# Optimization experiments

Measured on AMD Instinct MI355X. Metric: run time of the kernel, lower is better.

## Reference

```python
import jax, jax.numpy as jnp
import numpy as np

B, H, W, C, S, ITERS = 32, 80, 80, 32, 9, 3
HW = H * W
SCALE = C ** -0.5


def _grid(h, w):
    # matches SoftPositionEmbedding.build_grid: [1, h, w, 4] = [g, 1-g]
    r = jnp.stack(jnp.meshgrid(jnp.linspace(0., 1., h), jnp.linspace(0., 1., w), indexing='ij'), -1)
    return jnp.concatenate([r, 1. - r], -1)[None].astype(jnp.float32)


def _ln(x, g, b, ax):
    m = x.mean(ax, keepdims=True)
    v = x.var(ax, keepdims=True)
    return (x - m) / jnp.sqrt(v + 1e-5) * g + b


def _conv(x, w, b, p):
    y = jax.lax.conv_general_dilated(x, w, (1, 1), [(p, p), (p, p)],
                                     dimension_numbers=('NCHW', 'OIHW', 'NCHW'))
    return y + b[None, :, None, None]


def _convT(x, w, b, p):
    # stride-1 ConvTranspose2d == conv with spatially flipped kernel, pad k-1-p; w is [I,O,kh,kw]
    k = w.shape[-1]
    q = k - 1 - p
    y = jax.lax.conv_general_dilated(x, jnp.flip(w, (2, 3)), (1, 1), [(q, q), (q, q)],
                                     dimension_numbers=('NCHW', 'IOHW', 'NCHW'))
    return y + b[None, :, None, None]


def setup_inputs() -> dict:
    key = jax.random.key(0)
    ks = iter(jax.random.split(key, 64))

    def n(sh, s=0.05):
        return jax.random.normal(next(ks), sh, jnp.float32) * s

    return dict(
        x=jax.random.normal(next(ks), (B, 1, H, W), jnp.float32),
        slot_noise=jax.random.normal(next(ks), (B, S, C), jnp.float32),
        enc_w1=n((C, 1, 5, 5)), enc_b1=jnp.zeros((C,)),
        enc_w2=n((C, C, 5, 5)), enc_b2=jnp.zeros((C,)),
        enc_w3=n((C, C, 5, 5)), enc_b3=jnp.zeros((C,)),
        enc_w4=n((C, C, 5, 5)), enc_b4=jnp.zeros((C,)),
        pe_enc_w=n((C, 4)), pe_enc_b=jnp.zeros((C,)),
        ln_enc_g=jnp.ones((HW, C)), ln_enc_b=jnp.zeros((HW, C)),
        mlp_w1=n((C, C)), mlp_b1=jnp.zeros((C,)),
        mlp_w2=n((C, C)), mlp_b2=jnp.zeros((C,)),
        slots_mu=n((1, 1, C), 1.0), slots_sigma=jnp.abs(n((1, 1, C), 1.0)),
        ni_g=jnp.ones((C,)), ni_b=jnp.zeros((C,)),
        ns_g=jnp.ones((C,)), ns_b=jnp.zeros((C,)),
        q_w=n((C, C)), q_b=jnp.zeros((C,)),
        k_w=n((C, C)), k_b=jnp.zeros((C,)),
        v_w=n((C, C)), v_b=jnp.zeros((C,)),
        gru_wih=n((3 * C, C)), gru_whh=n((3 * C, C)),
        gru_bih=jnp.zeros((3 * C,)), gru_bhh=jnp.zeros((3 * C,)),
        res_ln_g=jnp.ones((C,)), res_ln_b=jnp.zeros((C,)),
        res_w1=n((C, C)), res_b1=jnp.zeros((C,)),
        res_w2=n((C, C)), res_b2=jnp.zeros((C,)),
        pe_dec_w=n((C, 4)), pe_dec_b=jnp.zeros((C,)),
        dec_w1=n((C, C, 5, 5)), dec_b1=jnp.zeros((C,)),
        dec_w2=n((C, C, 5, 5)), dec_b2=jnp.zeros((C,)),
        dec_w3=n((C, C, 5, 5)), dec_b3=jnp.zeros((C,)),
        dec_w4=n((C, 2, 3, 3)), dec_b4=jnp.zeros((2,)),
    )


def _forward(x, slot_noise, enc_w1, enc_b1, enc_w2, enc_b2, enc_w3, enc_b3, enc_w4, enc_b4,
             pe_enc_w, pe_enc_b, ln_enc_g, ln_enc_b, mlp_w1, mlp_b1, mlp_w2, mlp_b2,
             slots_mu, slots_sigma, ni_g, ni_b, ns_g, ns_b, q_w, q_b, k_w, k_b, v_w, v_b,
             gru_wih, gru_whh, gru_bih, gru_bhh, res_ln_g, res_ln_b, res_w1, res_b1,
             res_w2, res_b2, pe_dec_w, pe_dec_b, dec_w1, dec_b1, dec_w2, dec_b2,
             dec_w3, dec_b3, dec_w4, dec_b4):
    grid = _grid(H, W)  # [1,H,W,4]
    # --- conv encoder ---
    h = jax.nn.relu(_conv(x, enc_w1, enc_b1, 2))
    h = jax.nn.relu(_conv(h, enc_w2, enc_b2, 2))
    h = jax.nn.relu(_conv(h, enc_w3, enc_b3, 2))
    h = jax.nn.relu(_conv(h, enc_w4, enc_b4, 2))
    h = h.transpose(0, 2, 3, 1) + (grid @ pe_enc_w.T + pe_enc_b)  # soft pos emb
    h = h.reshape(B, HW, C)
    h = _ln(h, ln_enc_g, ln_enc_b, (-2, -1))  # LayerNorm([HW, C]): joint over last 2 dims
    h = jax.nn.relu(h @ mlp_w1.T + mlp_b1) @ mlp_w2.T + mlp_b2
    # --- slot attention ---
    slots = slots_mu + slots_sigma * slot_noise  # torch.normal(mu, sigma)
    xn = _ln(h, ni_g, ni_b, -1)
    keys = xn @ k_w.T + k_b
    values = xn @ v_w.T + v_b
    attn = None
    for _ in range(ITERS):
        prev = slots
        sn = _ln(slots, ns_g, ns_b, -1)
        q = sn @ q_w.T + q_b
        dots = jnp.einsum('bid,bjd->bij', q, keys) * SCALE  # [B,S,HW]
        attn = jax.nn.softmax(dots, axis=1) + 1e-8  # softmax over slots
        attn = attn / attn.sum(-1, keepdims=True)
        upd = jnp.einsum('bjd,bij->bid', values, attn)  # [B,S,C]
        # PyTorch GRUCell
        u2 = upd.reshape(-1, C)
        h2 = prev.reshape(-1, C)
        gx = u2 @ gru_wih.T + gru_bih
        gh = h2 @ gru_whh.T + gru_bhh
        xr, xz, xc = jnp.split(gx, 3, -1)
        hr, hz, hc = jnp.split(gh, 3, -1)
        r = jax.nn.sigmoid(xr + hr)
        z = jax.nn.sigmoid(xz + hz)
        cand = jnp.tanh(xc + r * hc)
        slots = ((1. - z) * cand + z * h2).reshape(B, S, C)
        res = _ln(slots, res_ln_g, res_ln_b, -1)
        res = jax.nn.relu(res @ res_w1.T + res_b1) @ res_w2.T + res_b2
        slots = slots + res
    # --- spatial-broadcast decoder ---
    d = jnp.broadcast_to(slots.reshape(B * S, 1, 1, C), (B * S, H, W, C))
    d = d + (grid @ pe_dec_w.T + pe_dec_b)
    d = d.transpose(0, 3, 1, 2)
    d = jax.nn.relu(_convT(d, dec_w1, dec_b1, 2))
    d = jax.nn.relu(_convT(d, dec_w2, dec_b2, 2))
    d = jax.nn.relu(_convT(d, dec_w3, dec_b3, 2))
    d = _convT(d, dec_w4, dec_b4, 1)
    d = d.transpose(0, 2, 3, 1).reshape(B, S, H, W, 2)
    recon, mlog = d[..., :1], d[..., 1:]
    mask = jax.nn.softmax(mlog, axis=1)  # over slots
    combined = (recon * mask).sum(1).transpose(0, 3, 1, 2)  # [B,1,H,W]
    return (combined, recon.transpose(0, 1, 4, 2, 3), mask.transpose(0, 1, 4, 2, 3),
            slots, attn.reshape(B, S, 1, H, W))


def reference(x, slot_noise, enc_w1, enc_b1, enc_w2, enc_b2, enc_w3, enc_b3, enc_w4, enc_b4,
              pe_enc_w, pe_enc_b, ln_enc_g, ln_enc_b, mlp_w1, mlp_b1, mlp_w2, mlp_b2,
              slots_mu, slots_sigma, ni_g, ni_b, ns_g, ns_b, q_w, q_b, k_w, k_b, v_w, v_b,
              gru_wih, gru_whh, gru_bih, gru_bhh, res_ln_g, res_ln_b, res_w1, res_b1,
              res_w2, res_b2, pe_dec_w, pe_dec_b, dec_w1, dec_b1, dec_w2, dec_b2,
              dec_w3, dec_b3, dec_w4, dec_b4):
    return _forward(x, slot_noise, enc_w1, enc_b1, enc_w2, enc_b2, enc_w3, enc_b3, enc_w4, enc_b4,
                    pe_enc_w, pe_enc_b, ln_enc_g, ln_enc_b, mlp_w1, mlp_b1, mlp_w2, mlp_b2,
                    slots_mu, slots_sigma, ni_g, ni_b, ns_g, ns_b, q_w, q_b, k_w, k_b, v_w, v_b,
                    gru_wih, gru_whh, gru_bih, gru_bhh, res_ln_g, res_ln_b, res_w1, res_b1,
                    res_w2, res_b2, pe_dec_w, pe_dec_b, dec_w1, dec_b1, dec_w2, dec_b2,
                    dec_w3, dec_b3, dec_w4, dec_b4)
```

## Files before the change

### kernel.cpp

```cpp
#include <hip/hip_runtime.h>
#include <cstddef>
#include <cstdint>


namespace {

constexpr int Bb  = 32;
constexpr int HWp = 6400;
constexpr float SCALEf = 0.17677669529663687f;

constexpr size_t O_COMB  = 0;
constexpr size_t O_RECON = 204800;
constexpr size_t O_MASK  = 2048000;
constexpr size_t O_SLOTS = 3891200;
constexpr size_t O_ATTN  = 3900416;

constexpr size_t W_PEENC = 0;
constexpr size_t W_PEDEC = 204800;
constexpr size_t W_BASE  = 409600;
constexpr size_t W_TC    = 512000;
constexpr size_t W_TS    = 537600;
constexpr size_t W_WP    = 768000;
constexpr size_t W_WPM   = 844800;
constexpr size_t W_LNPART= 846848;
constexpr size_t W_MEANR = 848448;
constexpr size_t W_Q     = 848512;
constexpr size_t W_SLOTS = 857728;
constexpr size_t W_APART = 866944;
constexpr size_t W_RSUM  = 874144;
constexpr size_t W_UP2   = 874432;
constexpr size_t W_KEYS  = 1104832;
constexpr size_t W_VALS  = 4381632;
constexpr size_t W_POOL  = 7658432;
constexpr size_t W_TOTAL = 29115328;

typedef __attribute__((ext_vector_type(8))) short short8;
typedef __attribute__((ext_vector_type(4))) float f32x4;

__device__ __forceinline__ ushort f2bf(float f) {
  uint u = __builtin_bit_cast(uint, f);
  uint r = (u + 0x7fffu + ((u >> 16) & 1u)) >> 16;
  return (ushort)r;
}
__device__ __forceinline__ float bf2f(ushort b) {
  uint u = ((uint)b) << 16;
  return __builtin_bit_cast(float, u);
}
__device__ __forceinline__ void unpk2(uint w, float& a, float& b) {
  a = __builtin_bit_cast(float, w << 16);
  b = __builtin_bit_cast(float, w & 0xffff0000u);
}

__device__ __forceinline__ float lane_ln(float v, int o, const float* __restrict__ g,
                                         const float* __restrict__ b) {
  float s = v;
#pragma unroll
  for (int m = 16; m >= 1; m >>= 1) s += __shfl_xor(s, m);
  float mean = s * (1.f / 32.f);
  float d = v - mean;
  float q = d * d;
#pragma unroll
  for (int m = 16; m >= 1; m >>= 1) q += __shfl_xor(q, m);
  float rstd = rsqrtf(q * (1.f / 32.f) + 1e-5f);
  return d * rstd * g[o] + b[o];
}


__global__ void k_pe_maps(const float* __restrict__ pew_e, const float* __restrict__ peb_e,
                          const float* __restrict__ pew_d, const float* __restrict__ peb_d,
                          float* __restrict__ pe_enc, float* __restrict__ pe_dec) {
  int hw = blockIdx.x * 256 + threadIdx.x;
  if (hw >= HWp) return;
  int y = hw / 80, x = hw % 80;
  float g0 = y * (1.f / 79.f), g1 = x * (1.f / 79.f);
  float g2 = 1.f - g0, g3 = 1.f - g1;
#pragma unroll
  for (int c = 0; c < 32; ++c) {
    pe_enc[(size_t)hw * 32 + c] = peb_e[c] + g0 * pew_e[c * 4] + g1 * pew_e[c * 4 + 1] +
                                  g2 * pew_e[c * 4 + 2] + g3 * pew_e[c * 4 + 3];
    pe_dec[(size_t)c * HWp + hw] = peb_d[c] + g0 * pew_d[c * 4] + g1 * pew_d[c * 4 + 1] +
                                   g2 * pew_d[c * 4 + 2] + g3 * pew_d[c * 4 + 3];
  }
}


__global__ void k_pack(const float* __restrict__ w, ushort* __restrict__ dst, int trans) {
  int tap = blockIdx.x;
  int grp = threadIdx.x >> 6, lane = threadIdx.x & 63;
  int ky = tap / 5, kx = tap % 5;
  int m = grp * 16 + (lane & 15);
  int kb = (lane >> 4) * 8;
  ushort* o = dst + ((size_t)(tap * 2 + grp) * 64 + lane) * 8;
#pragma unroll
  for (int j = 0; j < 8; ++j) {
    int k = kb + j;
    float v = trans ? w[(size_t)k * 800 + m * 25 + (4 - ky) * 5 + (4 - kx)]
                    : w[(size_t)m * 800 + k * 25 + ky * 5 + kx];
    o[j] = f2bf(v);
  }
}

__global__ void k_pack_mat(const float* __restrict__ w, ushort* __restrict__ dst) {
  int grp = threadIdx.x >> 6, lane = threadIdx.x & 63;
  int m = grp * 16 + (lane & 15), kb = (lane >> 4) * 8;
  ushort* o = dst + ((size_t)(grp * 64 + lane)) * 8;
#pragma unroll
  for (int j = 0; j < 8; ++j) o[j] = f2bf(w[m * 32 + kb + j]);
}


__global__ void k_prep_tc(const float* __restrict__ w, float* __restrict__ tc) {
  const int rep[5] = {0, 1, 40, 78, 79};
  int cls = blockIdx.x;
  int yc = cls / 5, xc = cls % 5;
  int ci = threadIdx.x >> 5, co = threadIdx.x & 31;
  int yr = rep[yc], xr = rep[xc];
  float s = 0.f;
#pragma unroll
  for (int ky = 0; ky < 5; ++ky) {
    if ((unsigned)(yr + ky - 2) >= 80u) continue;
#pragma unroll
    for (int kx = 0; kx < 5; ++kx) {
      if ((unsigned)(xr + kx - 2) >= 80u) continue;
      s += w[(size_t)ci * 800 + co * 25 + (4 - ky) * 5 + (4 - kx)];
    }
  }
  tc[(size_t)cls * 1024 + ci * 32 + co] = s;
}

__global__ void k_ts(const float* __restrict__ tc, const float* __restrict__ slots,
                     float* __restrict__ ts) {
  int idx = blockIdx.x * 256 + threadIdx.x;
  if (idx >= 288 * 800) return;
  int img = idx / 800, rem = idx % 800;
  int cls = rem >> 5, o = rem & 31;
  float s = 0.f;
#pragma unroll
  for (int ci = 0; ci < 32; ++ci)
    s += tc[(size_t)cls * 1024 + ci * 32 + o] * slots[(size_t)img * 32 + ci];
  ts[idx] = s;
}


template <int MODE, bool RELU>
__global__ __launch_bounds__(256, 4) void k_conv_mfma(
    const void* __restrict__ in_, const ushort* __restrict__ wp,
    const float* __restrict__ bias, ushort* __restrict__ out_,
    const float* __restrict__ ts, int n0) {
  __shared__ int4 sm[1600];
  const int n = blockIdx.y;
  const int ty = blockIdx.x / 5, tx = blockIdx.x % 5;
  const int t = threadIdx.x;

  for (int i = t; i < 1600; i += 256) {
    int u = i & 3, px = i >> 2;
    int x = px % 20, r = px / 20;
    int gy = ty * 16 + r - 2, gx = tx * 16 + x - 2;
    int4 pk = {0, 0, 0, 0};
    if ((unsigned)gy < 80u && (unsigned)gx < 80u) {
      int hw = gy * 80 + gx;
      if constexpr (MODE == 0) {
        const float* fp = (const float*)in_;
        ushort bb[8];
#pragma unroll
        for (int j = 0; j < 8; ++j)
          bb[j] = f2bf(fp[(size_t)(u * 8 + j) * HWp + hw]);
        pk.x = (int)((uint)bb[0] | ((uint)bb[1] << 16));
        pk.y = (int)((uint)bb[2] | ((uint)bb[3] << 16));
        pk.z = (int)((uint)bb[4] | ((uint)bb[5] << 16));
        pk.w = (int)((uint)bb[6] | ((uint)bb[7] << 16));
      } else if constexpr (MODE == 1) {
        pk = *(const int4*)((const ushort*)in_ + ((size_t)n * HWp + hw) * 32 + u * 8);
      } else {
        int4 bp = *(const int4*)((const ushort*)in_ + (size_t)hw * 32 + u * 8);
        int yc = gy < 2 ? gy : (gy > 77 ? gy - 75 : 2);
        int xc = gx < 2 ? gx : (gx > 77 ? gx - 75 : 2);
        const float* tp = ts + ((size_t)(n0 + n) * 25 + (yc * 5 + xc)) * 32 + u * 8;
        float t0, t1;
        uint* pw = (uint*)&pk;
        const uint* bw = (const uint*)&bp;
#pragma unroll
        for (int h = 0; h < 4; ++h) {
          unpk2(bw[h], t0, t1);
          float f0 = fmaxf(t0 + tp[2 * h], 0.f);
          float f1 = fmaxf(t1 + tp[2 * h + 1], 0.f);
          pw[h] = (uint)f2bf(f0) | ((uint)f2bf(f1) << 16);
        }
      }
    }
    int up = u ^ ((x >> 1) & 3);
    sm[(r * 20 + x) * 4 + up] = pk;
  }
  __syncthreads();

  const int wv = t >> 6, lane = t & 63;
  const int l15 = lane & 15, lg = lane >> 4;
  const short8* smS = (const short8*)sm;

  f32x4 acc[4][2];
#pragma unroll
  for (int o = 0; o < 4; ++o)
#pragma unroll
    for (int c = 0; c < 2; ++c) acc[o][c] = f32x4{0.f, 0.f, 0.f, 0.f};

#pragma unroll
  for (int dx = 0; dx < 5; ++dx) {
    short8 Adx[5][2];
#pragma unroll
    for (int dy = 0; dy < 5; ++dy) {
      int tap = dy * 5 + dx;
      Adx[dy][0] = *(const short8*)(wp + ((size_t)(tap * 2 + 0) * 64 + lane) * 8);
      Adx[dy][1] = *(const short8*)(wp + ((size_t)(tap * 2 + 1) * 64 + lane) * 8);
    }
    const int xx = l15 + dx;
    const int us = lg ^ ((xx >> 1) & 3);
#pragma unroll
    for (int r8 = 0; r8 < 8; ++r8) {
      short8 Bv = smS[((wv * 4 + r8) * 20 + xx) * 4 + us];
#pragma unroll
      for (int o = 0; o < 4; ++o) {
        int dy = r8 - o;
        if (dy < 0 || dy > 4) continue;
        acc[o][0] = __builtin_amdgcn_mfma_f32_16x16x32_bf16(Adx[dy][0], Bv, acc[o][0], 0, 0, 0);
        acc[o][1] = __builtin_amdgcn_mfma_f32_16x16x32_bf16(Adx[dy][1], Bv, acc[o][1], 0, 0, 0);
      }
    }
  }

  float bv[2][4];
#pragma unroll
  for (int cg = 0; cg < 2; ++cg)
#pragma unroll
    for (int q = 0; q < 4; ++q) bv[cg][q] = bias[cg * 16 + lg * 4 + q];
  const int ybase = ty * 16 + wv * 4, xbase = tx * 16 + l15;
#pragma unroll
  for (int o = 0; o < 4; ++o) {
    size_t px = (size_t)n * HWp + (ybase + o) * 80 + xbase;
#pragma unroll
    for (int cg = 0; cg < 2; ++cg) {
      f32x4 v = acc[o][cg];
      float o0 = v[0] + bv[cg][0], o1 = v[1] + bv[cg][1];
      float o2 = v[2] + bv[cg][2], o3 = v[3] + bv[cg][3];
      if (RELU) {
        o0 = fmaxf(o0, 0.f); o1 = fmaxf(o1, 0.f);
        o2 = fmaxf(o2, 0.f); o3 = fmaxf(o3, 0.f);
      }
      uint2 pk;
      pk.x = (uint)f2bf(o0) | ((uint)f2bf(o1) << 16);
      pk.y = (uint)f2bf(o2) | ((uint)f2bf(o3) << 16);
      *(uint2*)(out_ + px * 32 + cg * 16 + lg * 4) = pk;
    }
  }
}


__global__ __launch_bounds__(256) void k_conv1(const float* __restrict__ in,
                                               const float* __restrict__ w,
                                               const float* __restrict__ b,
                                               ushort* __restrict__ out) {
  int hw = blockIdx.x * 256 + threadIdx.x;
  int n = blockIdx.y;
  int y = hw / 80, x = hw % 80;
  float xv[25];
#pragma unroll
  for (int ky = 0; ky < 5; ++ky)
#pragma unroll
    for (int kx = 0; kx < 5; ++kx) {
      int iy = y + ky - 2, ix = x + kx - 2;
      xv[ky * 5 + kx] = ((unsigned)iy < 80u && (unsigned)ix < 80u)
                            ? in[(size_t)n * HWp + iy * 80 + ix] : 0.f;
    }
  float a[32];
#pragma unroll
  for (int co = 0; co < 32; ++co) {
    float s = b[co];
#pragma unroll
    for (int tp = 0; tp < 25; ++tp) s = fmaf(xv[tp], w[co * 25 + tp], s);
    a[co] = fmaxf(s, 0.f);
  }
  ushort* op = out + ((size_t)n * HWp + hw) * 32;
#pragma unroll
  for (int g = 0; g < 4; ++g) {
    uint4 pk;
    pk.x = (uint)f2bf(a[g * 8 + 0]) | ((uint)f2bf(a[g * 8 + 1]) << 16);
    pk.y = (uint)f2bf(a[g * 8 + 2]) | ((uint)f2bf(a[g * 8 + 3]) << 16);
    pk.z = (uint)f2bf(a[g * 8 + 4]) | ((uint)f2bf(a[g * 8 + 5]) << 16);
    pk.w = (uint)f2bf(a[g * 8 + 6]) | ((uint)f2bf(a[g * 8 + 7]) << 16);
    *(uint4*)(op + g * 8) = pk;
  }
}


__global__ __launch_bounds__(256) void k_conv4(const ushort* __restrict__ in,
                                               const float* __restrict__ w,
                                               const float* __restrict__ b,
                                               float* __restrict__ outR,
                                               float* __restrict__ outM, int n0) {
  __shared__ float sw[2 * 288];
  for (int e = threadIdx.x; e < 576; e += 256) {
    int co = e / 288, rem = e % 288;
    int tap = rem / 32, ci = rem % 32;
    sw[e] = w[(size_t)(ci * 2 + co) * 9 + 8 - tap];
  }
  __syncthreads();
  int hw = blockIdx.x * 256 + threadIdx.x;
  int nl = blockIdx.y;
  int y = hw / 80, x = hw % 80;
  float a0 = b[0], a1 = b[1];
  const ushort* ip = in + (size_t)nl * HWp * 32;
#pragma unroll
  for (int ky = 0; ky < 3; ++ky) {
#pragma unroll
    for (int kx = 0; kx < 3; ++kx) {
      int iy = y + ky - 1, ix = x + kx - 1;
      if ((unsigned)iy >= 80u || (unsigned)ix >= 80u) continue;
      int tap = ky * 3 + kx;
      const int4* p = (const int4*)(ip + (size_t)(iy * 80 + ix) * 32);
      const float* w0 = sw + tap * 32;
      const float* w1 = sw + 288 + tap * 32;
#pragma unroll
      for (int u = 0; u < 4; ++u) {
        int4 ch = p[u];
        const uint* cw = (const uint*)&ch;
#pragma unroll
        for (int h = 0; h < 4; ++h) {
          float v0, v1;
          unpk2(cw[h], v0, v1);
          int ci = u * 8 + h * 2;
          a0 = fmaf(v0, w0[ci], a0);     a1 = fmaf(v0, w1[ci], a1);
          a0 = fmaf(v1, w0[ci + 1], a0); a1 = fmaf(v1, w1[ci + 1], a1);
        }
      }
    }
  }
  outR[(size_t)(n0 + nl) * HWp + hw] = a0;
  outM[(size_t)(n0 + nl) * HWp + hw] = a1;
}


__global__ __launch_bounds__(256) void k_hstats(const ushort* __restrict__ enc,
                                                const float* __restrict__ pe_enc,
                                                float* __restrict__ lnpart) {
  int b = blockIdx.y;
  int hw = blockIdx.x * 256 + threadIdx.x;
  const int4* ep = (const int4*)(enc + ((size_t)b * HWp + hw) * 32);
  float v[32];
#pragma unroll
  for (int u = 0; u < 4; ++u) {
    int4 ch = ep[u];
    const uint* cw = (const uint*)&ch;
#pragma unroll
    for (int h = 0; h < 4; ++h) unpk2(cw[h], v[u * 8 + h * 2], v[u * 8 + h * 2 + 1]);
  }
  float s = 0.f, ss = 0.f;
#pragma unroll
  for (int c = 0; c < 32; ++c) {
    v[c] += pe_enc[(size_t)hw * 32 + c];
    s += v[c]; ss += v[c] * v[c];
  }
  __shared__ float r1[256], r2[256];
  r1[threadIdx.x] = s; r2[threadIdx.x] = ss;
  __syncthreads();
  for (int off = 128; off > 0; off >>= 1) {
    if (threadIdx.x < off) { r1[threadIdx.x] += r1[threadIdx.x + off]; r2[threadIdx.x] += r2[threadIdx.x + off]; }
    __syncthreads();
  }
  if (threadIdx.x == 0) {
    lnpart[(size_t)(b * 25 + blockIdx.x) * 2] = r1[0];
    lnpart[(size_t)(b * 25 + blockIdx.x) * 2 + 1] = r2[0];
  }
}

__global__ void k_statsfin(const float* __restrict__ lnpart, float* __restrict__ meanr) {
  int b = threadIdx.x;
  if (b >= 32) return;
  float s = 0.f, ss = 0.f;
  for (int k = 0; k < 25; ++k) {
    s += lnpart[(size_t)(b * 25 + k) * 2];
    ss += lnpart[(size_t)(b * 25 + k) * 2 + 1];
  }
  float m = s * (1.f / 204800.f);
  float var = ss * (1.f / 204800.f) - m * m;
  meanr[b * 2] = m;
  meanr[b * 2 + 1] = rsqrtf(var + 1e-5f);
}


__global__ __launch_bounds__(256) void k_lnmlpkv_mfma(
    const ushort* __restrict__ enc, const float* __restrict__ pe,
    const float* __restrict__ meanr,
    const float* __restrict__ g, const float* __restrict__ bb,
    const ushort* __restrict__ wm,
    const float* __restrict__ b1, const float* __restrict__ b2,
    const float* __restrict__ nig, const float* __restrict__ nib,
    const float* __restrict__ kb, const float* __restrict__ vb,
    ushort* __restrict__ keys, ushort* __restrict__ vals) {
  __shared__ ushort ls[256 * 32];
  const int b = blockIdx.y, jb = blockIdx.x;
  const int t = threadIdx.x, wv = t >> 6, lane = t & 63;
  const int l15 = lane & 15, lg = lane >> 4;
  const int skey = l15 & 3;

  short8 A[4][2];
#pragma unroll
  for (int mt = 0; mt < 4; ++mt)
#pragma unroll
    for (int gr = 0; gr < 2; ++gr)
      A[mt][gr] = *(const short8*)(wm + ((size_t)(mt * 2 + gr) * 64 + lane) * 8);

  float4 b1v0 = *(const float4*)(b1 + lg * 4),  b1v1 = *(const float4*)(b1 + 16 + lg * 4);
  float4 b2v0 = *(const float4*)(b2 + lg * 4),  b2v1 = *(const float4*)(b2 + 16 + lg * 4);
  float4 ng0  = *(const float4*)(nig + lg * 4), ng1  = *(const float4*)(nig + 16 + lg * 4);
  float4 nb0  = *(const float4*)(nib + lg * 4), nb1  = *(const float4*)(nib + 16 + lg * 4);
  float4 kbv0 = *(const float4*)(kb + lg * 4),  kbv1 = *(const float4*)(kb + 16 + lg * 4);
  float4 vbv0 = *(const float4*)(vb + lg * 4),  vbv1 = *(const float4*)(vb + 16 + lg * 4);

  const float m_ = meanr[b * 2], rs_ = meanr[b * 2 + 1];

  short8 bx[4];
#pragma unroll
  for (int g2 = 0; g2 < 4; ++g2) {
    int pos = jb * 256 + wv * 64 + g2 * 16 + l15;
    int4 e = *(const int4*)(enc + ((size_t)b * HWp + pos) * 32 + lg * 8);
    float xv[8];
    const uint* ew = (const uint*)&e;
#pragma unroll
    for (int h = 0; h < 4; ++h) unpk2(ew[h], xv[2 * h], xv[2 * h + 1]);
    float4 p0 = *(const float4*)(pe + (size_t)pos * 32 + lg * 8);
    float4 p1 = *(const float4*)(pe + (size_t)pos * 32 + lg * 8 + 4);
    float4 g0 = *(const float4*)(g + (size_t)pos * 32 + lg * 8);
    float4 g1 = *(const float4*)(g + (size_t)pos * 32 + lg * 8 + 4);
    float4 q0 = *(const float4*)(bb + (size_t)pos * 32 + lg * 8);
    float4 q1 = *(const float4*)(bb + (size_t)pos * 32 + lg * 8 + 4);
    float pv[8] = {p0.x, p0.y, p0.z, p0.w, p1.x, p1.y, p1.z, p1.w};
    float gv[8] = {g0.x, g0.y, g0.z, g0.w, g1.x, g1.y, g1.z, g1.w};
    float qv[8] = {q0.x, q0.y, q0.z, q0.w, q1.x, q1.y, q1.z, q1.w};
    uint pk[4];
#pragma unroll
    for (int h = 0; h < 4; ++h) {
      float f0 = (xv[2 * h] + pv[2 * h] - m_) * rs_ * gv[2 * h] + qv[2 * h];
      float f1 = (xv[2 * h + 1] + pv[2 * h + 1] - m_) * rs_ * gv[2 * h + 1] + qv[2 * h + 1];
      pk[h] = (uint)f2bf(f0) | ((uint)f2bf(f1) << 16);
    }
    bx[g2] = __builtin_bit_cast(short8, *(int4*)pk);
  }

  auto lds_write = [&](int posl, int cg, const f32x4& v) {
    int u = cg * 2 + (lg >> 1);
    int us = u ^ skey;
    uint2 pk;
    pk.x = (uint)f2bf(v[0]) | ((uint)f2bf(v[1]) << 16);
    pk.y = (uint)f2bf(v[2]) | ((uint)f2bf(v[3]) << 16);
    *(uint2*)(ls + (size_t)posl * 32 + us * 8 + (lg & 1) * 4) = pk;
  };

#pragma unroll
  for (int g2 = 0; g2 < 4; ++g2) {
    int posl = wv * 64 + g2 * 16 + l15;
    f32x4 a0 = __builtin_amdgcn_mfma_f32_16x16x32_bf16(A[0][0], bx[g2], f32x4{0, 0, 0, 0}, 0, 0, 0);
    f32x4 a1 = __builtin_amdgcn_mfma_f32_16x16x32_bf16(A[0][1], bx[g2], f32x4{0, 0, 0, 0}, 0, 0, 0);
    f32x4 r0, r1;
#pragma unroll
    for (int q = 0; q < 4; ++q) {
      r0[q] = fmaxf(a0[q] + (&b1v0.x)[q], 0.f);
      r1[q] = fmaxf(a1[q] + (&b1v1.x)[q], 0.f);
    }
    lds_write(posl, 0, r0);
    lds_write(posl, 1, r1);
  }
  __syncthreads();
  short8 t0f[4];
#pragma unroll
  for (int g2 = 0; g2 < 4; ++g2) {
    int posl = wv * 64 + g2 * 16 + l15;
    t0f[g2] = *(const short8*)(ls + (size_t)posl * 32 + (lg ^ skey) * 8);
  }
  __syncthreads();

#pragma unroll
  for (int g2 = 0; g2 < 4; ++g2) {
    int posl = wv * 64 + g2 * 16 + l15;
    f32x4 c0 = __builtin_amdgcn_mfma_f32_16x16x32_bf16(A[1][0], t0f[g2], f32x4{0, 0, 0, 0}, 0, 0, 0);
    f32x4 c1 = __builtin_amdgcn_mfma_f32_16x16x32_bf16(A[1][1], t0f[g2], f32x4{0, 0, 0, 0}, 0, 0, 0);
#pragma unroll
    for (int q = 0; q < 4; ++q) { c0[q] += (&b2v0.x)[q]; c1[q] += (&b2v1.x)[q]; }
    float s = 0.f;
#pragma unroll
    for (int q = 0; q < 4; ++q) s += c0[q] + c1[q];
    s += __shfl_xor(s, 16); s += __shfl_xor(s, 32);
    float mean = s * (1.f / 32.f);
    float var = 0.f;
#pragma unroll
    for (int q = 0; q < 4; ++q) {
      float d0 = c0[q] - mean, d1 = c1[q] - mean;
      var += d0 * d0 + d1 * d1;
    }
    var += __shfl_xor(var, 16); var += __shfl_xor(var, 32);
    float rstd = rsqrtf(var * (1.f / 32.f) + 1e-5f);
    f32x4 y0, y1;
#pragma unroll
    for (int q = 0; q < 4; ++q) {
      y0[q] = (c0[q] - mean) * rstd * (&ng0.x)[q] + (&nb0.x)[q];
      y1[q] = (c1[q] - mean) * rstd * (&ng1.x)[q] + (&nb1.x)[q];
    }
    lds_write(posl, 0, y0);
    lds_write(posl, 1, y1);
  }
  __syncthreads();
  short8 xnf[4];
#pragma unroll
  for (int g2 = 0; g2 < 4; ++g2) {
    int posl = wv * 64 + g2 * 16 + l15;
    xnf[g2] = *(const short8*)(ls + (size_t)posl * 32 + (lg ^ skey) * 8);
  }

#pragma unroll
  for (int g2 = 0; g2 < 4; ++g2) {
    int pos = jb * 256 + wv * 64 + g2 * 16 + l15;
    size_t px = ((size_t)b * HWp + pos) * 32;
    f32x4 k0 = __builtin_amdgcn_mfma_f32_16x16x32_bf16(A[2][0], xnf[g2], f32x4{0, 0, 0, 0}, 0, 0, 0);
    f32x4 k1 = __builtin_amdgcn_mfma_f32_16x16x32_bf16(A[2][1], xnf[g2], f32x4{0, 0, 0, 0}, 0, 0, 0);
    f32x4 v0 = __builtin_amdgcn_mfma_f32_16x16x32_bf16(A[3][0], xnf[g2], f32x4{0, 0, 0, 0}, 0, 0, 0);
    f32x4 v1 = __builtin_amdgcn_mfma_f32_16x16x32_bf16(A[3][1], xnf[g2], f32x4{0, 0, 0, 0}, 0, 0, 0);
    uint2 pk;
    pk.x = (uint)f2bf(k0[0] + kbv0.x) | ((uint)f2bf(k0[1] + kbv0.y) << 16);
    pk.y = (uint)f2bf(k0[2] + kbv0.z) | ((uint)f2bf(k0[3] + kbv0.w) << 16);
    *(uint2*)(keys + px + lg * 4) = pk;
    pk.x = (uint)f2bf(k1[0] + kbv1.x) | ((uint)f2bf(k1[1] + kbv1.y) << 16);
    pk.y = (uint)f2bf(k1[2] + kbv1.z) | ((uint)f2bf(k1[3] + kbv1.w) << 16);
    *(uint2*)(keys + px + 16 + lg * 4) = pk;
    pk.x = (uint)f2bf(v0[0] + vbv0.x) | ((uint)f2bf(v0[1] + vbv0.y) << 16);
    pk.y = (uint)f2bf(v0[2] + vbv0.z) | ((uint)f2bf(v0[3] + vbv0.w) << 16);
    *(uint2*)(vals + px + lg * 4) = pk;
    pk.x = (uint)f2bf(v1[0] + vbv1.x) | ((uint)f2bf(v1[1] + vbv1.y) << 16);
    pk.y = (uint)f2bf(v1[2] + vbv1.z) | ((uint)f2bf(v1[3] + vbv1.w) << 16);
    *(uint2*)(vals + px + 16 + lg * 4) = pk;
  }
}


__global__ __launch_bounds__(256) void k_init_q(
    const float* __restrict__ mu, const float* __restrict__ sig,
    const float* __restrict__ noise,
    const float* __restrict__ nsg, const float* __restrict__ nsb,
    const float* __restrict__ qw, const float* __restrict__ qb,
    float* __restrict__ slots, float* __restrict__ qbuf) {
  int rl = threadIdx.x >> 5, o = threadIdx.x & 31;
  int r = blockIdx.x * 8 + rl;
  float s = mu[o] + sig[o] * noise[(size_t)r * 32 + o];
  slots[(size_t)r * 32 + o] = s;
  float y = lane_ln(s, o, nsg, nsb);
  __shared__ float S[8][32];
  S[rl][o] = y;
  __syncthreads();
  float qv = qb[o];
#pragma unroll
  for (int c = 0; c < 32; ++c) qv = fmaf(S[rl][c], qw[o * 32 + c], qv);
  qbuf[(size_t)r * 32 + o] = qv;
}

template <bool LAST>
__global__ __launch_bounds__(256) void k_dots_upd(
    const float* __restrict__ qbuf, const ushort* __restrict__ keys,
    const ushort* __restrict__ vals, float* __restrict__ attnt,
    float* __restrict__ apart, float* __restrict__ up2) {
  int b = blockIdx.y, jb = blockIdx.x;
  int t = threadIdx.x;
  int j = jb * 256 + t;
  __shared__ float qs[288];
  __shared__ float aL[2304];
  __shared__ float wr[36];
  for (int e = t; e < 288; e += 256) qs[e] = qbuf[(size_t)b * 288 + e];
  __syncthreads();
  float k[32];
  const int4* kp = (const int4*)(keys + ((size_t)b * HWp + j) * 32);
#pragma unroll
  for (int u = 0; u < 4; ++u) {
    int4 ch = kp[u];
    const uint* cw = (const uint*)&ch;
#pragma unroll
    for (int h = 0; h < 4; ++h) unpk2(cw[h], k[u * 8 + h * 2], k[u * 8 + h * 2 + 1]);
  }
  float d[9];
#pragma unroll
  for (int i = 0; i < 9; ++i) {
    float a = 0.f;
#pragma unroll
    for (int c = 0; c < 32; ++c) a = fmaf(qs[i * 32 + c], k[c], a);
    d[i] = a * SCALEf;
  }
  float mx = d[0];
#pragma unroll
  for (int i = 1; i < 9; ++i) mx = fmaxf(mx, d[i]);
  float sum = 0.f;
#pragma unroll
  for (int i = 0; i < 9; ++i) { d[i] = __expf(d[i] - mx); sum += d[i]; }
  float inv = 1.f / sum;
  float a9[9];
#pragma unroll
  for (int i = 0; i < 9; ++i) {
    a9[i] = d[i] * inv + 1e-8f;
    if (LAST) attnt[((size_t)b * 9 + i) * HWp + j] = a9[i];
    aL[t * 9 + i] = a9[i];
  }
  int lane = t & 63, wid = t >> 6;
#pragma unroll
  for (int i = 0; i < 9; ++i) {
    float v = a9[i];
    for (int off = 32; off > 0; off >>= 1) v += __shfl_down(v, off);
    if (lane == 0) wr[wid * 9 + i] = v;
  }
  __syncthreads();
  if (t < 9)
    apart[(size_t)(b * 9 + t) * 25 + jb] = wr[t] + wr[9 + t] + wr[18 + t] + wr[27 + t];
  int c = t & 31, g = t >> 5;
  float acc[9];
#pragma unroll
  for (int i = 0; i < 9; ++i) acc[i] = 0.f;
  const ushort* vp = vals + ((size_t)b * HWp + jb * 256) * 32 + c;
  for (int jj = g; jj < 256; jj += 8) {
    float v = bf2f(vp[(size_t)jj * 32]);
#pragma unroll
    for (int i = 0; i < 9; ++i) acc[i] = fmaf(v, aL[jj * 9 + i], acc[i]);
  }
  __syncthreads();
#pragma unroll
  for (int i = 0; i < 9; ++i) aL[(i * 8 + g) * 32 + c] = acc[i];
  __syncthreads();
  for (int i = g; i < 9; i += 8) {
    float s = 0.f;
#pragma unroll
    for (int g2 = 0; g2 < 8; ++g2) s += aL[(i * 8 + g2) * 32 + c];
    up2[(((size_t)b * 25 + jb) * 9 + i) * 32 + c] = s;
  }
}

__global__ __launch_bounds__(256) void k_gru_fused(
    const float* __restrict__ up2, const float* __restrict__ apart,
    float* __restrict__ slots, float* __restrict__ rowsum, float* __restrict__ qbuf,
    const float* __restrict__ wih, const float* __restrict__ whh,
    const float* __restrict__ bih, const float* __restrict__ bhh,
    const float* __restrict__ rlg, const float* __restrict__ rlb,
    const float* __restrict__ rw1, const float* __restrict__ rb1,
    const float* __restrict__ rw2, const float* __restrict__ rb2,
    const float* __restrict__ nsg, const float* __restrict__ nsb,
    const float* __restrict__ qw, const float* __restrict__ qb) {
  int rl = threadIdx.x >> 5, o = threadIdx.x & 31;
  int r = blockIdx.x * 8 + rl;
  int b = r / 9, i = r - b * 9;

  float rs = 0.f;
#pragma unroll
  for (int k = 0; k < 25; ++k) rs += apart[(size_t)(b * 9 + i) * 25 + k];
  if (o == 0) rowsum[r] = rs;

  float uo = 0.f;
#pragma unroll
  for (int jc = 0; jc < 25; ++jc) uo += up2[(((size_t)b * 25 + jc) * 9 + i) * 32 + o];
  uo /= rs;
  float ho = slots[(size_t)r * 32 + o];

  __shared__ float Us[8][32], Hs[8][32];
  Us[rl][o] = uo; Hs[rl][o] = ho;
  __syncthreads();

  float xr = bih[o], xz = bih[32 + o], xc = bih[64 + o];
  float hr = bhh[o], hz = bhh[32 + o], hc = bhh[64 + o];
#pragma unroll
  for (int c = 0; c < 32; ++c) {
    float u = Us[rl][c], h = Hs[rl][c];
    xr = fmaf(u, wih[o * 32 + c], xr);          hr = fmaf(h, whh[o * 32 + c], hr);
    xz = fmaf(u, wih[(32 + o) * 32 + c], xz);   hz = fmaf(h, whh[(32 + o) * 32 + c], hz);
    xc = fmaf(u, wih[(64 + o) * 32 + c], xc);   hc = fmaf(h, whh[(64 + o) * 32 + c], hc);
  }
  float rr = 1.f / (1.f + __expf(-(xr + hr)));
  float zz = 1.f / (1.f + __expf(-(xz + hz)));
  float cand = tanhf(xc + rr * hc);
  float sm = (1.f - zz) * cand + zz * ho;

  float y = lane_ln(sm, o, rlg, rlb);
  __syncthreads();
  Us[rl][o] = y;
  __syncthreads();
  float t1 = rb1[o];
#pragma unroll
  for (int c = 0; c < 32; ++c) t1 = fmaf(Us[rl][c], rw1[o * 32 + c], t1);
  t1 = fmaxf(t1, 0.f);
  Hs[rl][o] = t1;
  __syncthreads();
  float res = rb2[o];
#pragma unroll
  for (int c = 0; c < 32; ++c) res = fmaf(Hs[rl][c], rw2[o * 32 + c], res);
  float ns = sm + res;
  slots[(size_t)r * 32 + o] = ns;

  float y2 = lane_ln(ns, o, nsg, nsb);
  __syncthreads();
  Us[rl][o] = y2;
  __syncthreads();
  float qv = qb[o];
#pragma unroll
  for (int c = 0; c < 32; ++c) qv = fmaf(Us[rl][c], qw[o * 32 + c], qv);
  qbuf[(size_t)r * 32 + o] = qv;
}


__global__ void k_attn_out(const float* __restrict__ attnt, const float* __restrict__ rsum,
                           float* __restrict__ out) {
  size_t idx = (size_t)blockIdx.x * 256 + threadIdx.x;
  out[O_ATTN + idx] = attnt[idx] / rsum[idx / HWp];
}

__global__ void k_slots_out(const float* __restrict__ slots, float* __restrict__ out) {
  int idx = blockIdx.x * 256 + threadIdx.x;
  if (idx < 9216) out[O_SLOTS + idx] = slots[idx];
}

__global__ __launch_bounds__(256) void k_final(float* __restrict__ out) {
  int b = blockIdx.y;
  int j = blockIdx.x * 256 + threadIdx.x;
  float r[9], ml[9];
#pragma unroll
  for (int s = 0; s < 9; ++s) {
    r[s]  = out[O_RECON + (size_t)(b * 9 + s) * HWp + j];
    ml[s] = out[O_MASK  + (size_t)(b * 9 + s) * HWp + j];
  }
  float mx = ml[0];
#pragma unroll
  for (int s = 1; s < 9; ++s) mx = fmaxf(mx, ml[s]);
  float sum = 0.f;
#pragma unroll
  for (int s = 0; s < 9; ++s) { ml[s] = __expf(ml[s] - mx); sum += ml[s]; }
  float inv = 1.f / sum;
  float comb = 0.f;
#pragma unroll
  for (int s = 0; s < 9; ++s) {
    float mk = ml[s] * inv;
    comb = fmaf(r[s], mk, comb);
    out[O_MASK + (size_t)(b * 9 + s) * HWp + j] = mk;
  }
  out[O_COMB + (size_t)b * HWp + j] = comb;
}

}


extern "C" void kernel_launch(void* const* d_in, const int* in_sizes, int n_in,
                              void* d_out, int out_size, void* d_ws, size_t ws_size,
                              hipStream_t stream) {
  if (ws_size < W_TOTAL * sizeof(float)) return;

  const float* in_x       = (const float*)d_in[0];
  const float* slot_noise = (const float*)d_in[1];
  const float* enc_w1 = (const float*)d_in[2];   const float* enc_b1 = (const float*)d_in[3];
  const float* enc_w2 = (const float*)d_in[4];   const float* enc_b2 = (const float*)d_in[5];
  const float* enc_w3 = (const float*)d_in[6];   const float* enc_b3 = (const float*)d_in[7];
  const float* enc_w4 = (const float*)d_in[8];   const float* enc_b4 = (const float*)d_in[9];
  const float* pe_enc_w = (const float*)d_in[10]; const float* pe_enc_b = (const float*)d_in[11];
  const float* ln_enc_g = (const float*)d_in[12]; const float* ln_enc_b = (const float*)d_in[13];
  const float* mlp_w1 = (const float*)d_in[14];  const float* mlp_b1 = (const float*)d_in[15];
  const float* mlp_w2 = (const float*)d_in[16];  const float* mlp_b2 = (const float*)d_in[17];
  const float* slots_mu = (const float*)d_in[18]; const float* slots_sigma = (const float*)d_in[19];
  const float* ni_g = (const float*)d_in[20];    const float* ni_b = (const float*)d_in[21];
  const float* ns_g = (const float*)d_in[22];    const float* ns_b = (const float*)d_in[23];
  const float* q_w = (const float*)d_in[24];     const float* q_b = (const float*)d_in[25];
  const float* k_w = (const float*)d_in[26];     const float* k_b = (const float*)d_in[27];
  const float* v_w = (const float*)d_in[28];     const float* v_b = (const float*)d_in[29];
  const float* gru_wih = (const float*)d_in[30]; const float* gru_whh = (const float*)d_in[31];
  const float* gru_bih = (const float*)d_in[32]; const float* gru_bhh = (const float*)d_in[33];
  const float* res_ln_g = (const float*)d_in[34]; const float* res_ln_b = (const float*)d_in[35];
  const float* res_w1 = (const float*)d_in[36];  const float* res_b1 = (const float*)d_in[37];
  const float* res_w2 = (const float*)d_in[38];  const float* res_b2 = (const float*)d_in[39];
  const float* pe_dec_w = (const float*)d_in[40]; const float* pe_dec_b = (const float*)d_in[41];
  const float* dec_w1 = (const float*)d_in[42];  const float* dec_b1 = (const float*)d_in[43];
  const float* dec_w2 = (const float*)d_in[44];  const float* dec_b2 = (const float*)d_in[45];
  const float* dec_w3 = (const float*)d_in[46];  const float* dec_b3 = (const float*)d_in[47];
  const float* dec_w4 = (const float*)d_in[48];  const float* dec_b4 = (const float*)d_in[49];

  float* ws  = (float*)d_ws;
  float* out = (float*)d_out;
  ushort* wp  = (ushort*)(ws + W_WP);
  ushort* wpm = (ushort*)(ws + W_WPM);

  k_pe_maps<<<dim3(25), 256, 0, stream>>>(pe_enc_w, pe_enc_b, pe_dec_w, pe_dec_b,
                                          ws + W_PEENC, ws + W_PEDEC);

  const size_t WPSTR = 25 * 2 * 64 * 8;
  k_pack<<<dim3(25), 128, 0, stream>>>(enc_w2, wp + 0 * WPSTR, 0);
  k_pack<<<dim3(25), 128, 0, stream>>>(enc_w3, wp + 1 * WPSTR, 0);
  k_pack<<<dim3(25), 128, 0, stream>>>(enc_w4, wp + 2 * WPSTR, 0);
  k_pack<<<dim3(25), 128, 0, stream>>>(dec_w1, wp + 3 * WPSTR, 1);
  k_pack<<<dim3(25), 128, 0, stream>>>(dec_w2, wp + 4 * WPSTR, 1);
  k_pack<<<dim3(25), 128, 0, stream>>>(dec_w3, wp + 5 * WPSTR, 1);
  k_pack_mat<<<dim3(1), 128, 0, stream>>>(mlp_w1, wpm + 0 * 1024);
  k_pack_mat<<<dim3(1), 128, 0, stream>>>(mlp_w2, wpm + 1 * 1024);
  k_pack_mat<<<dim3(1), 128, 0, stream>>>(k_w,   wpm + 2 * 1024);
  k_pack_mat<<<dim3(1), 128, 0, stream>>>(v_w,   wpm + 3 * 1024);
  k_prep_tc<<<dim3(25), 1024, 0, stream>>>(dec_w1, ws + W_TC);

  ushort* base  = (ushort*)(ws + W_BASE);
  ushort* keys  = (ushort*)(ws + W_KEYS);
  ushort* vals  = (ushort*)(ws + W_VALS);
  float*  attnt = ws + W_POOL;
  ushort* E1    = (ushort*)(ws + W_POOL);
  ushort* E2    = (ushort*)(ws + W_POOL + 3276800);

  k_conv_mfma<0, false><<<dim3(25, 1), 256, 0, stream>>>(
      ws + W_PEDEC, wp + 3 * WPSTR, dec_b1, base, nullptr, 0);

  k_conv1<<<dim3(25, Bb), 256, 0, stream>>>(in_x, enc_w1, enc_b1, E1);
  k_conv_mfma<1, true><<<dim3(25, Bb), 256, 0, stream>>>(E1, wp + 0 * WPSTR, enc_b2, E2, nullptr, 0);
  k_conv_mfma<1, true><<<dim3(25, Bb), 256, 0, stream>>>(E2, wp + 1 * WPSTR, enc_b3, E1, nullptr, 0);
  k_conv_mfma<1, true><<<dim3(25, Bb), 256, 0, stream>>>(E1, wp + 2 * WPSTR, enc_b4, E2, nullptr, 0);

  k_hstats<<<dim3(25, Bb), 256, 0, stream>>>(E2, ws + W_PEENC, ws + W_LNPART);
  k_statsfin<<<dim3(1), 64, 0, stream>>>(ws + W_LNPART, ws + W_MEANR);
  k_lnmlpkv_mfma<<<dim3(25, Bb), 256, 0, stream>>>(E2, ws + W_PEENC, ws + W_MEANR,
                                                   ln_enc_g, ln_enc_b, wpm,
                                                   mlp_b1, mlp_b2, ni_g, ni_b,
                                                   k_b, v_b, keys, vals);

  k_init_q<<<dim3(36), 256, 0, stream>>>(slots_mu, slots_sigma, slot_noise,
                                         ns_g, ns_b, q_w, q_b, ws + W_SLOTS, ws + W_Q);
  for (int it = 0; it < 3; ++it) {
    if (it == 2)
      k_dots_upd<true><<<dim3(25, Bb), 256, 0, stream>>>(ws + W_Q, keys, vals, attnt,
                                                         ws + W_APART, ws + W_UP2);
    else
      k_dots_upd<false><<<dim3(25, Bb), 256, 0, stream>>>(ws + W_Q, keys, vals, attnt,
                                                          ws + W_APART, ws + W_UP2);
    k_gru_fused<<<dim3(36), 256, 0, stream>>>(ws + W_UP2, ws + W_APART,
                                              ws + W_SLOTS, ws + W_RSUM, ws + W_Q,
                                              gru_wih, gru_whh, gru_bih, gru_bhh,
                                              res_ln_g, res_ln_b, res_w1, res_b1,
                                              res_w2, res_b2, ns_g, ns_b, q_w, q_b);
  }
  k_attn_out<<<dim3(7200), 256, 0, stream>>>(attnt, ws + W_RSUM, out);
  k_slots_out<<<dim3(36), 256, 0, stream>>>(ws + W_SLOTS, out);

  k_ts<<<dim3(900), 256, 0, stream>>>(ws + W_TC, ws + W_SLOTS, ws + W_TS);

  ushort* XA = (ushort*)(ws + W_POOL);
  ushort* XB = XA + (size_t)96 * 32 * HWp;
  for (int ch = 0; ch < 3; ++ch) {
    int n0 = ch * 96;
    k_conv_mfma<2, true><<<dim3(25, 96), 256, 0, stream>>>(base, wp + 4 * WPSTR, dec_b2, XA,
                                                           ws + W_TS, n0);
    k_conv_mfma<1, true><<<dim3(25, 96), 256, 0, stream>>>(XA, wp + 5 * WPSTR, dec_b3, XB,
                                                           nullptr, 0);
    k_conv4<<<dim3(25, 96), 256, 0, stream>>>(XB, dec_w4, dec_b4,
                                              out + O_RECON, out + O_MASK, n0);
  }

  k_final<<<dim3(25, Bb), 256, 0, stream>>>(out);
}
```

Baseline: 565.4 us.

## Store intermediate activations in zero-padded layout and read conv inputs directly

Intermediate bf16 activation buffers now use an 84x84 layout with a zero border. This lets a new direct conv kernel read its B operands straight from global memory, with no LDS staging, halo bounds checks or swizzle. Downstream consumers (conv4, hstats, LN/MLP) are changed to index the padded layout, and the decoder batch chunking goes from 3x96 to 4x72 to fit the larger buffers. The cost is extra border-zeroing launches and global reads of overlapping windows that hit cache instead of LDS reuse.

New measurement: 649.6 us. 1.15x slower.

```diff
diff --git a/kernel.cpp b/kernel.cpp
--- a/kernel.cpp
+++ b/kernel.cpp
@@ -7,6 +7,8 @@
 
 constexpr int Bb  = 32;
 constexpr int HWp = 6400;
+constexpr int PW  = 84;
+constexpr int PHW = 7056;
 constexpr float SCALEf = 0.17677669529663687f;
 
 constexpr size_t O_COMB  = 0;
@@ -84,6 +86,19 @@
 }
 
 
+__global__ void k_zero_border(ushort* __restrict__ buf, int nimg) {
+  int i = blockIdx.x * 256 + threadIdx.x;
+  if (i >= nimg * 656) return;
+  int img = i / 656, e = i % 656;
+  int y, x;
+  if (e < 336) { int r = e / 84; y = (r < 2) ? r : 80 + r; x = e % 84; }
+  else { int rem = e - 336; y = 2 + rem / 4; int c = rem % 4; x = (c < 2) ? c : 80 + c; }
+  int4* p = (int4*)(buf + ((size_t)img * PHW + y * PW + x) * 32);
+  int4 z = {0, 0, 0, 0};
+  p[0] = z; p[1] = z; p[2] = z; p[3] = z;
+}
+
+
 __global__ void k_pack(const float* __restrict__ w, ushort* __restrict__ dst, int trans) {
   int tap = blockIdx.x;
   int grp = threadIdx.x >> 6, lane = threadIdx.x & 63;
@@ -142,7 +157,74 @@
 }
 
 
-template <int MODE, bool RELU>
+template <bool RELU>
+__global__ __launch_bounds__(256, 4) void k_conv_direct(
+    const ushort* __restrict__ in, const ushort* __restrict__ wp,
+    const float* __restrict__ bias, ushort* __restrict__ out) {
+  const int n = blockIdx.y;
+  const int ty = blockIdx.x / 5, tx = blockIdx.x % 5;
+  const int t = threadIdx.x, wv = t >> 6, lane = t & 63;
+  const int l15 = lane & 15, lg = lane >> 4;
+
+  const ushort* ib = in + ((size_t)n * PHW + (ty * 16 + wv * 4) * PW + tx * 16 + l15) * 32 + lg * 8;
+
+  f32x4 acc[4][2];
+#pragma unroll
+  for (int o = 0; o < 4; ++o)
+#pragma unroll
+    for (int c = 0; c < 2; ++c) acc[o][c] = f32x4{0.f, 0.f, 0.f, 0.f};
+
+#pragma unroll
+  for (int dx = 0; dx < 5; ++dx) {
+    short8 Adx[5][2];
+#pragma unroll
+    for (int dy = 0; dy < 5; ++dy) {
+      int tap = dy * 5 + dx;
+      Adx[dy][0] = *(const short8*)(wp + ((size_t)(tap * 2 + 0) * 64 + lane) * 8);
+      Adx[dy][1] = *(const short8*)(wp + ((size_t)(tap * 2 + 1) * 64 + lane) * 8);
+    }
+    const ushort* bcol = ib + (size_t)dx * 32;
+#pragma unroll
+    for (int r8 = 0; r8 < 8; ++r8) {
+      short8 Bv = *(const short8*)(bcol + (size_t)r8 * (PW * 32));
+#pragma unroll
+      for (int o = 0; o < 4; ++o) {
+        int dy = r8 - o;
+        if (dy < 0 || dy > 4) continue;
+        acc[o][0] = __builtin_amdgcn_mfma_f32_16x16x32_bf16(Adx[dy][0], Bv, acc[o][0], 0, 0, 0);
+        acc[o][1] = __builtin_amdgcn_mfma_f32_16x16x32_bf16(Adx[dy][1], Bv, acc[o][1], 0, 0, 0);
+      }
+    }
+  }
+
+  float bv[2][4];
+#pragma unroll
+  for (int cg = 0; cg < 2; ++cg)
+#pragma unroll
+    for (int q = 0; q < 4; ++q) bv[cg][q] = bias[cg * 16 + lg * 4 + q];
+  const int ybase = ty * 16 + wv * 4, xbase = tx * 16 + l15;
+#pragma unroll
+  for (int o = 0; o < 4; ++o) {
+    size_t px = (size_t)n * PHW + (ybase + o + 2) * PW + (xbase + 2);
+#pragma unroll
+    for (int cg = 0; cg < 2; ++cg) {
+      f32x4 v = acc[o][cg];
+      float o0 = v[0] + bv[cg][0], o1 = v[1] + bv[cg][1];
+      float o2 = v[2] + bv[cg][2], o3 = v[3] + bv[cg][3];
+      if (RELU) {
+        o0 = fmaxf(o0, 0.f); o1 = fmaxf(o1, 0.f);
+        o2 = fmaxf(o2, 0.f); o3 = fmaxf(o3, 0.f);
+      }
+      uint2 pk;
+      pk.x = (uint)f2bf(o0) | ((uint)f2bf(o1) << 16);
+      pk.y = (uint)f2bf(o2) | ((uint)f2bf(o3) << 16);
+      *(uint2*)(out + px * 32 + cg * 16 + lg * 4) = pk;
+    }
+  }
+}
+
+
+template <int MODE, bool RELU, bool PADOUT>
 __global__ __launch_bounds__(256, 4) void k_conv_mfma(
     const void* __restrict__ in_, const ushort* __restrict__ wp,
     const float* __restrict__ bias, ushort* __restrict__ out_,
@@ -169,8 +251,6 @@
         pk.y = (int)((uint)bb[2] | ((uint)bb[3] << 16));
         pk.z = (int)((uint)bb[4] | ((uint)bb[5] << 16));
         pk.w = (int)((uint)bb[6] | ((uint)bb[7] << 16));
-      } else if constexpr (MODE == 1) {
-        pk = *(const int4*)((const ushort*)in_ + ((size_t)n * HWp + hw) * 32 + u * 8);
       } else {
         int4 bp = *(const int4*)((const ushort*)in_ + (size_t)hw * 32 + u * 8);
         int yc = gy < 2 ? gy : (gy > 77 ? gy - 75 : 2);
@@ -235,7 +315,9 @@
   const int ybase = ty * 16 + wv * 4, xbase = tx * 16 + l15;
 #pragma unroll
   for (int o = 0; o < 4; ++o) {
-    size_t px = (size_t)n * HWp + (ybase + o) * 80 + xbase;
+    size_t px;
+    if (PADOUT) px = (size_t)n * PHW + (ybase + o + 2) * PW + (xbase + 2);
+    else        px = (size_t)n * HWp + (ybase + o) * 80 + xbase;
 #pragma unroll
     for (int cg = 0; cg < 2; ++cg) {
       f32x4 v = acc[o][cg];
@@ -278,7 +360,7 @@
     for (int tp = 0; tp < 25; ++tp) s = fmaf(xv[tp], w[co * 25 + tp], s);
     a[co] = fmaxf(s, 0.f);
   }
-  ushort* op = out + ((size_t)n * HWp + hw) * 32;
+  ushort* op = out + ((size_t)n * PHW + (y + 2) * PW + x + 2) * 32;
 #pragma unroll
   for (int g = 0; g < 4; ++g) {
     uint4 pk;
@@ -307,15 +389,13 @@
   int nl = blockIdx.y;
   int y = hw / 80, x = hw % 80;
   float a0 = b[0], a1 = b[1];
-  const ushort* ip = in + (size_t)nl * HWp * 32;
+  const ushort* ip = in + (size_t)nl * PHW * 32;
 #pragma unroll
   for (int ky = 0; ky < 3; ++ky) {
 #pragma unroll
     for (int kx = 0; kx < 3; ++kx) {
-      int iy = y + ky - 1, ix = x + kx - 1;
-      if ((unsigned)iy >= 80u || (unsigned)ix >= 80u) continue;
       int tap = ky * 3 + kx;
-      const int4* p = (const int4*)(ip + (size_t)(iy * 80 + ix) * 32);
+      const int4* p = (const int4*)(ip + (size_t)((y + ky + 1) * PW + x + kx + 1) * 32);
       const float* w0 = sw + tap * 32;
       const float* w1 = sw + 288 + tap * 32;
 #pragma unroll
@@ -343,7 +423,8 @@
                                                 float* __restrict__ lnpart) {
   int b = blockIdx.y;
   int hw = blockIdx.x * 256 + threadIdx.x;
-  const int4* ep = (const int4*)(enc + ((size_t)b * HWp + hw) * 32);
+  int y = hw / 80, x = hw % 80;
+  const int4* ep = (const int4*)(enc + ((size_t)b * PHW + (y + 2) * PW + x + 2) * 32);
   float v[32];
 #pragma unroll
   for (int u = 0; u < 4; ++u) {
@@ -421,7 +502,8 @@
 #pragma unroll
   for (int g2 = 0; g2 < 4; ++g2) {
     int pos = jb * 256 + wv * 64 + g2 * 16 + l15;
-    int4 e = *(const int4*)(enc + ((size_t)b * HWp + pos) * 32 + lg * 8);
+    int y = pos / 80, x = pos % 80;
+    int4 e = *(const int4*)(enc + ((size_t)b * PHW + (y + 2) * PW + x + 2) * 32 + lg * 8);
     float xv[8];
     const uint* ew = (const uint*)&e;
 #pragma unroll
@@ -803,15 +885,18 @@
   ushort* vals  = (ushort*)(ws + W_VALS);
   float*  attnt = ws + W_POOL;
   ushort* E1    = (ushort*)(ws + W_POOL);
-  ushort* E2    = (ushort*)(ws + W_POOL + 3276800);
-
-  k_conv_mfma<0, false><<<dim3(25, 1), 256, 0, stream>>>(
+  ushort* E2    = (ushort*)(ws + W_POOL + 3612672);
+
+  k_conv_mfma<0, false, false><<<dim3(25, 1), 256, 0, stream>>>(
       ws + W_PEDEC, wp + 3 * WPSTR, dec_b1, base, nullptr, 0);
 
+  k_zero_border<<<dim3((32 * 656 + 255) / 256), 256, 0, stream>>>(E1, 32);
+  k_zero_border<<<dim3((32 * 656 + 255) / 256), 256, 0, stream>>>(E2, 32);
+
   k_conv1<<<dim3(25, Bb), 256, 0, stream>>>(in_x, enc_w1, enc_b1, E1);
-  k_conv_mfma<1, true><<<dim3(25, Bb), 256, 0, stream>>>(E1, wp + 0 * WPSTR, enc_b2, E2, nullptr, 0);
-  k_conv_mfma<1, true><<<dim3(25, Bb), 256, 0, stream>>>(E2, wp + 1 * WPSTR, enc_b3, E1, nullptr, 0);
-  k_conv_mfma<1, true><<<dim3(25, Bb), 256, 0, stream>>>(E1, wp + 2 * WPSTR, enc_b4, E2, nullptr, 0);
+  k_conv_direct<true><<<dim3(25, Bb), 256, 0, stream>>>(E1, wp + 0 * WPSTR, enc_b2, E2);
+  k_conv_direct<true><<<dim3(25, Bb), 256, 0, stream>>>(E2, wp + 1 * WPSTR, enc_b3, E1);
+  k_conv_direct<true><<<dim3(25, Bb), 256, 0, stream>>>(E1, wp + 2 * WPSTR, enc_b4, E2);
 
   k_hstats<<<dim3(25, Bb), 256, 0, stream>>>(E2, ws + W_PEENC, ws + W_LNPART);
   k_statsfin<<<dim3(1), 64, 0, stream>>>(ws + W_LNPART, ws + W_MEANR);
@@ -841,14 +926,15 @@
   k_ts<<<dim3(900), 256, 0, stream>>>(ws + W_TC, ws + W_SLOTS, ws + W_TS);
 
   ushort* XA = (ushort*)(ws + W_POOL);
-  ushort* XB = XA + (size_t)96 * 32 * HWp;
-  for (int ch = 0; ch < 3; ++ch) {
-    int n0 = ch * 96;
-    k_conv_mfma<2, true><<<dim3(25, 96), 256, 0, stream>>>(base, wp + 4 * WPSTR, dec_b2, XA,
-                                                           ws + W_TS, n0);
-    k_conv_mfma<1, true><<<dim3(25, 96), 256, 0, stream>>>(XA, wp + 5 * WPSTR, dec_b3, XB,
-                                                           nullptr, 0);
-    k_conv4<<<dim3(25, 96), 256, 0, stream>>>(XB, dec_w4, dec_b4,
+  ushort* XB = (ushort*)(ws + W_POOL + 8128512);
+  k_zero_border<<<dim3((72 * 656 + 255) / 256), 256, 0, stream>>>(XA, 72);
+  k_zero_border<<<dim3((72 * 656 + 255) / 256), 256, 0, stream>>>(XB, 72);
+  for (int ch = 0; ch < 4; ++ch) {
+    int n0 = ch * 72;
+    k_conv_mfma<2, true, true><<<dim3(25, 72), 256, 0, stream>>>(base, wp + 4 * WPSTR, dec_b2,
+                                                                 XA, ws + W_TS, n0);
+    k_conv_direct<true><<<dim3(25, 72), 256, 0, stream>>>(XA, wp + 5 * WPSTR, dec_b3, XB);
+    k_conv4<<<dim3(25, 72), 256, 0, stream>>>(XB, dec_w4, dec_b4,
                                               out + O_RECON, out + O_MASK, n0);
   }
 
```

## Add double-buffered conv kernel processing two images per block for decoder conv3

Applied to the files above, without the earlier changes.

Adds a new MFMA conv kernel in which each block handles two images. The second image's global loads are issued into registers while the first image is being computed, then written to a second shared-memory buffer. It replaces the decoder's conv3 launch and halves the grid, with the aim of hiding global-load latency behind MFMA work. The cost is more register pressure (launch bounds of 256 threads with min 3 blocks, plus 7 int4 prefetch registers) and fewer blocks, which lowers parallelism.

Result: slower. 606.2 us (+7.2%).

```diff
diff --git a/kernel.cpp b/kernel.cpp
--- a/kernel.cpp
+++ b/kernel.cpp
@@ -251,6 +251,111 @@
       *(uint2*)(out_ + px * 32 + cg * 16 + lg * 4) = pk;
     }
   }
+}
+
+
+template <bool RELU>
+__global__ __launch_bounds__(256, 3) void k_conv_pipe(
+    const ushort* __restrict__ in, const ushort* __restrict__ wp,
+    const float* __restrict__ bias, ushort* __restrict__ out) {
+  __shared__ int4 sm[2][1600];
+  const int pr = blockIdx.y;
+  const int ty = blockIdx.x / 5, tx = blockIdx.x % 5;
+  const int t = threadIdx.x;
+  const int wv = t >> 6, lane = t & 63;
+  const int l15 = lane & 15, lg = lane >> 4;
+
+  auto load_img = [&](int bi, int4* rr) {
+#pragma unroll
+    for (int k = 0; k < 7; ++k) {
+      int e = t + (k << 8);
+      if (k < 6 || e < 1600) {
+        int u = e & 3, px = e >> 2;
+        int x = px % 20, r = px / 20;
+        int gy = ty * 16 + r - 2, gx = tx * 16 + x - 2;
+        int4 pk = {0, 0, 0, 0};
+        if ((unsigned)gy < 80u && (unsigned)gx < 80u)
+          pk = *(const int4*)(in + ((size_t)bi * HWp + gy * 80 + gx) * 32 + u * 8);
+        rr[k] = pk;
+      }
+    }
+  };
+  auto write_sm = [&](int buf, const int4* rr) {
+#pragma unroll
+    for (int k = 0; k < 7; ++k) {
+      int e = t + (k << 8);
+      if (k < 6 || e < 1600) {
+        int u = e & 3, px = e >> 2;
+        int x = px % 20, r = px / 20;
+        sm[buf][(r * 20 + x) * 4 + (u ^ ((x >> 1) & 3))] = rr[k];
+      }
+    }
+  };
+  auto compute_store = [&](int buf, int bi) {
+    const short8* smS = (const short8*)sm[buf];
+    f32x4 acc[4][2];
+#pragma unroll
+    for (int o = 0; o < 4; ++o)
+#pragma unroll
+      for (int c = 0; c < 2; ++c) acc[o][c] = f32x4{0.f, 0.f, 0.f, 0.f};
+#pragma unroll
+    for (int dx = 0; dx < 5; ++dx) {
+      short8 Adx[5][2];
+#pragma unroll
+      for (int dy = 0; dy < 5; ++dy) {
+        int tap = dy * 5 + dx;
+        Adx[dy][0] = *(const short8*)(wp + ((size_t)(tap * 2 + 0) * 64 + lane) * 8);
+        Adx[dy][1] = *(const short8*)(wp + ((size_t)(tap * 2 + 1) * 64 + lane) * 8);
+      }
+      const int xx = l15 + dx;
+      const int us = lg ^ ((xx >> 1) & 3);
+#pragma unroll
+      for (int r8 = 0; r8 < 8; ++r8) {
+        short8 Bv = smS[((wv * 4 + r8) * 20 + xx) * 4 + us];
+#pragma unroll
+        for (int o = 0; o < 4; ++o) {
+          int dy = r8 - o;
+          if (dy < 0 || dy > 4) continue;
+          acc[o][0] = __builtin_amdgcn_mfma_f32_16x16x32_bf16(Adx[dy][0], Bv, acc[o][0], 0, 0, 0);
+          acc[o][1] = __builtin_amdgcn_mfma_f32_16x16x32_bf16(Adx[dy][1], Bv, acc[o][1], 0, 0, 0);
+        }
+      }
+    }
+    float bvv[2][4];
+#pragma unroll
+    for (int cg = 0; cg < 2; ++cg)
+#pragma unroll
+      for (int q = 0; q < 4; ++q) bvv[cg][q] = bias[cg * 16 + lg * 4 + q];
+    const int ybase = ty * 16 + wv * 4, xbase = tx * 16 + l15;
+#pragma unroll
+    for (int o = 0; o < 4; ++o) {
+      size_t px = (size_t)bi * HWp + (ybase + o) * 80 + xbase;
+#pragma unroll
+      for (int cg = 0; cg < 2; ++cg) {
+        f32x4 v = acc[o][cg];
+        float o0 = v[0] + bvv[cg][0], o1 = v[1] + bvv[cg][1];
+        float o2 = v[2] + bvv[cg][2], o3 = v[3] + bvv[cg][3];
+        if (RELU) {
+          o0 = fmaxf(o0, 0.f); o1 = fmaxf(o1, 0.f);
+          o2 = fmaxf(o2, 0.f); o3 = fmaxf(o3, 0.f);
+        }
+        uint2 pk;
+        pk.x = (uint)f2bf(o0) | ((uint)f2bf(o1) << 16);
+        pk.y = (uint)f2bf(o2) | ((uint)f2bf(o3) << 16);
+        *(uint2*)(out + px * 32 + cg * 16 + lg * 4) = pk;
+      }
+    }
+  };
+
+  int4 rr[7];
+  load_img(pr * 2, rr);
+  write_sm(0, rr);
+  __syncthreads();
+  load_img(pr * 2 + 1, rr);
+  compute_store(0, pr * 2);
+  write_sm(1, rr);
+  __syncthreads();
+  compute_store(1, pr * 2 + 1);
 }
 
 
@@ -846,8 +951,7 @@
     int n0 = ch * 96;
     k_conv_mfma<2, true><<<dim3(25, 96), 256, 0, stream>>>(base, wp + 4 * WPSTR, dec_b2, XA,
                                                            ws + W_TS, n0);
-    k_conv_mfma<1, true><<<dim3(25, 96), 256, 0, stream>>>(XA, wp + 5 * WPSTR, dec_b3, XB,
-                                                           nullptr, 0);
+    k_conv_pipe<true><<<dim3(25, 48), 256, 0, stream>>>(XA, wp + 5 * WPSTR, dec_b3, XB);
     k_conv4<<<dim3(25, 96), 256, 0, stream>>>(XB, dec_w4, dec_b4,
                                               out + O_RECON, out + O_MASK, n0);
   }
```
